# Kernel optimization log

Measured on AMD Instinct MI355X. Metric: run time of the kernel, lower is better.

Reference implementation:

```python
import jax, jax.numpy as jnp
import numpy as np

B, C, IN, OUT = 2048, 64, 512, 512


def setup_inputs() -> dict:
    key = jax.random.key(0)
    k1, k2, k3 = jax.random.split(key, 3)
    x = jax.random.normal(k1, (B, IN), dtype=jnp.float32)
    index = jax.random.randint(k2, (B,), 0, C, dtype=jnp.int64)
    # kaiming_uniform-ish init: bound = sqrt(6 / ((1 + 5) * fan_in)) = 1/sqrt(fan_in)
    bound = 1.0 / np.sqrt(IN)
    weight = jax.random.uniform(k3, (C, OUT, IN), dtype=jnp.float32,
                                minval=-bound, maxval=bound)
    return {"input": x, "index": index, "weight": weight}


def reference(input, index, weight):
    # weight: (C, OUT, IN); index: (B,); input: (B, IN)
    w = weight[index]                      # (B, OUT, IN) gathered per-sample matrix
    return jnp.einsum('boi,bi->bo', w, input)  # batched matvec -> (B, OUT)
```

## Files before the change

kernel.cpp:

```cpp
#include <hip/hip_runtime.h>


constexpr int Bsz  = 2048;
constexpr int Ccnt = 64;
constexpr int INF  = 512;
constexpr int OUTF = 512;
constexpr int THREADS = 256;
constexpr int OT = 64;
constexpr int NT = 64;

typedef __attribute__((ext_vector_type(8))) short bf16x8;
typedef __attribute__((ext_vector_type(4))) float f32x4;

__device__ __forceinline__ unsigned short f2bf(float f) {
    union { float f; unsigned u; } v; v.f = f;
    return (unsigned short)((v.u + 0x7FFFu + ((v.u >> 16) & 1u)) >> 16);
}

__global__ __launch_bounds__(THREADS)
void switching_linear_kernel(const float* __restrict__ x,
                             const int* __restrict__ idx,
                             const float* __restrict__ w,
                             float* __restrict__ out) {
    __shared__ unsigned short list[Bsz];
    __shared__ int ls_n;

    const int tid = threadIdx.x;
    const int c  = blockIdx.x >> 3;
    const int o0 = (blockIdx.x & 7) * OT;

    if (tid == 0) ls_n = 0;
    __syncthreads();
    for (int i = tid; i < Bsz; i += THREADS) {
        if (idx[i] == c) list[atomicAdd(&ls_n, 1)] = (unsigned short)i;
    }
    __syncthreads();
    const int n = ls_n;
    if (n == 0) return;

    const int wave = tid >> 6;
    const int lane = tid & 63;
    const int mrow = lane & 15;
    const int quad = lane >> 4;
    const int ow   = o0 + wave * 16;

    const float* aptr = w + ((size_t)c * OUTF + (size_t)(ow + mrow)) * INF + quad * 8;

    for (int s0 = 0; s0 < n; s0 += NT) {
        const float* bptr[4];
        bool bval[4];
#pragma unroll
        for (int g = 0; g < 4; ++g) {
            int s = s0 + g * 16 + mrow;
            bval[g] = (s < n);
            int b = bval[g] ? (int)list[s] : 0;
            bptr[g] = x + (size_t)b * INF + quad * 8;
        }

        f32x4 acc[4] = {{0.f,0.f,0.f,0.f},{0.f,0.f,0.f,0.f},
                        {0.f,0.f,0.f,0.f},{0.f,0.f,0.f,0.f}};

#pragma unroll 2
        for (int kt = 0; kt < INF; kt += 32) {
            float4 a0 = *(const float4*)(aptr + kt);
            float4 a1 = *(const float4*)(aptr + kt + 4);
            bf16x8 af;
            af[0] = (short)f2bf(a0.x); af[1] = (short)f2bf(a0.y);
            af[2] = (short)f2bf(a0.z); af[3] = (short)f2bf(a0.w);
            af[4] = (short)f2bf(a1.x); af[5] = (short)f2bf(a1.y);
            af[6] = (short)f2bf(a1.z); af[7] = (short)f2bf(a1.w);

#pragma unroll
            for (int g = 0; g < 4; ++g) {
                bf16x8 bf = {0,0,0,0,0,0,0,0};
                if (bval[g]) {
                    float4 b0 = *(const float4*)(bptr[g] + kt);
                    float4 b1 = *(const float4*)(bptr[g] + kt + 4);
                    bf[0] = (short)f2bf(b0.x); bf[1] = (short)f2bf(b0.y);
                    bf[2] = (short)f2bf(b0.z); bf[3] = (short)f2bf(b0.w);
                    bf[4] = (short)f2bf(b1.x); bf[5] = (short)f2bf(b1.y);
                    bf[6] = (short)f2bf(b1.z); bf[7] = (short)f2bf(b1.w);
                }
                acc[g] = __builtin_amdgcn_mfma_f32_16x16x32_bf16(af, bf, acc[g], 0, 0, 0);
            }
        }

#pragma unroll
        for (int g = 0; g < 4; ++g) {
            int s = s0 + g * 16 + mrow;
            if (s < n) {
                int b = (int)list[s];
                float* dst = out + (size_t)b * OUTF + ow + quad * 4;
                *(float4*)dst = make_float4(acc[g][0], acc[g][1], acc[g][2], acc[g][3]);
            }
        }
    }
}

extern "C" void kernel_launch(void* const* d_in, const int* in_sizes, int n_in,
                              void* d_out, int out_size, void* d_ws, size_t ws_size,
                              hipStream_t stream) {
    const float* x   = (const float*)d_in[0];
    const int*   idx = (const int*)d_in[1];
    const float* w   = (const float*)d_in[2];
    float* out = (float*)d_out;

    dim3 grid(Ccnt * (OUTF / OT));
    dim3 block(THREADS);
    switching_linear_kernel<<<grid, block, 0, stream>>>(x, idx, w, out);
}
```

Measured before the change: 125.0 us.

## Split K across waves with LDS reduction, halve output tile, use packed bf16 convert

Halves the output tile per block (doubling the grid to 1024 blocks) and splits the K dimension across wave pairs, combining the two partial sums through shared memory before the store. It also swaps the manual bf16 rounding for a packed hardware conversion builtin when available, and skips MFMA groups that hold no valid samples in the tail tile. The aim is more parallelism and latency hiding for a memory-bound gather GEMM, at the cost of extra syncthreads and LDS traffic per sample tile.

```diff
diff --git a/kernel.cpp b/kernel.cpp
--- a/kernel.cpp
+++ b/kernel.cpp
@@ -6,28 +6,51 @@
 constexpr int INF  = 512;
 constexpr int OUTF = 512;
 constexpr int THREADS = 256;
-constexpr int OT = 64;
+constexpr int OT = 32;
 constexpr int NT = 64;
+constexpr int NBLK = Ccnt * (OUTF / OT);
 
 typedef __attribute__((ext_vector_type(8))) short bf16x8;
 typedef __attribute__((ext_vector_type(4))) float f32x4;
 
-__device__ __forceinline__ unsigned short f2bf(float f) {
+#if __has_builtin(__builtin_amdgcn_cvt_pk_bf16_f32)
+typedef __attribute__((ext_vector_type(2))) __bf16 bf16x2_t;
+__device__ __forceinline__ int cvt2i(float a, float b) {
+    union { bf16x2_t v; int i; } u;
+    u.v = __builtin_amdgcn_cvt_pk_bf16_f32(a, b);
+    return u.i;
+}
+#else
+__device__ __forceinline__ unsigned f2bf(float f) {
     union { float f; unsigned u; } v; v.f = f;
-    return (unsigned short)((v.u + 0x7FFFu + ((v.u >> 16) & 1u)) >> 16);
+    return (v.u + 0x7FFFu + ((v.u >> 16) & 1u)) >> 16;
+}
+__device__ __forceinline__ int cvt2i(float a, float b) {
+    return (int)(f2bf(a) | (f2bf(b) << 16));
+}
+#endif
+
+__device__ __forceinline__ bf16x8 cvt8(float4 a, float4 b) {
+    union { bf16x8 v; int i[4]; } u;
+    u.i[0] = cvt2i(a.x, a.y);
+    u.i[1] = cvt2i(a.z, a.w);
+    u.i[2] = cvt2i(b.x, b.y);
+    u.i[3] = cvt2i(b.z, b.w);
+    return u.v;
 }
 
-__global__ __launch_bounds__(THREADS)
+__global__ __launch_bounds__(THREADS, 4)
 void switching_linear_kernel(const float* __restrict__ x,
                              const int* __restrict__ idx,
                              const float* __restrict__ w,
                              float* __restrict__ out) {
     __shared__ unsigned short list[Bsz];
     __shared__ int ls_n;
+    __shared__ float red[2][16][64];
 
     const int tid = threadIdx.x;
-    const int c  = blockIdx.x >> 3;
-    const int o0 = (blockIdx.x & 7) * OT;
+    const int c  = blockIdx.x >> 4;
+    const int o0 = (blockIdx.x & 15) * OT;
 
     if (tid == 0) ls_n = 0;
     __syncthreads();
@@ -40,13 +63,20 @@
 
     const int wave = tid >> 6;
     const int lane = tid & 63;
+    const int r    = wave & 1;
+    const int kh   = wave >> 1;
     const int mrow = lane & 15;
     const int quad = lane >> 4;
-    const int ow   = o0 + wave * 16;
+    const int ow   = o0 + r * 16;
+    const int k0   = kh * (INF / 2);
 
-    const float* aptr = w + ((size_t)c * OUTF + (size_t)(ow + mrow)) * INF + quad * 8;
+    const float* aptr = w + ((size_t)c * OUTF + (size_t)(ow + mrow)) * INF
+                          + k0 + quad * 8;
 
     for (int s0 = 0; s0 < n; s0 += NT) {
+        const int rem = n - s0;
+        const int ng  = rem >= NT ? 4 : (rem + 15) >> 4;
+
         const float* bptr[4];
         bool bval[4];
 #pragma unroll
@@ -54,46 +84,57 @@
             int s = s0 + g * 16 + mrow;
             bval[g] = (s < n);
             int b = bval[g] ? (int)list[s] : 0;
-            bptr[g] = x + (size_t)b * INF + quad * 8;
+            bptr[g] = x + (size_t)b * INF + k0 + quad * 8;
         }
 
         f32x4 acc[4] = {{0.f,0.f,0.f,0.f},{0.f,0.f,0.f,0.f},
                         {0.f,0.f,0.f,0.f},{0.f,0.f,0.f,0.f}};
 
-#pragma unroll 2
-        for (int kt = 0; kt < INF; kt += 32) {
+#pragma unroll 4
+        for (int kt = 0; kt < INF / 2; kt += 32) {
             float4 a0 = *(const float4*)(aptr + kt);
             float4 a1 = *(const float4*)(aptr + kt + 4);
-            bf16x8 af;
-            af[0] = (short)f2bf(a0.x); af[1] = (short)f2bf(a0.y);
-            af[2] = (short)f2bf(a0.z); af[3] = (short)f2bf(a0.w);
-            af[4] = (short)f2bf(a1.x); af[5] = (short)f2bf(a1.y);
-            af[6] = (short)f2bf(a1.z); af[7] = (short)f2bf(a1.w);
+            bf16x8 af = cvt8(a0, a1);
 
-#pragma unroll
-            for (int g = 0; g < 4; ++g) {
-                bf16x8 bf = {0,0,0,0,0,0,0,0};
+            for (int g = 0; g < ng; ++g) {
+                bf16x8 bfr = {0,0,0,0,0,0,0,0};
                 if (bval[g]) {
                     float4 b0 = *(const float4*)(bptr[g] + kt);
                     float4 b1 = *(const float4*)(bptr[g] + kt + 4);
-                    bf[0] = (short)f2bf(b0.x); bf[1] = (short)f2bf(b0.y);
-                    bf[2] = (short)f2bf(b0.z); bf[3] = (short)f2bf(b0.w);
-                    bf[4] = (short)f2bf(b1.x); bf[5] = (short)f2bf(b1.y);
-                    bf[6] = (short)f2bf(b1.z); bf[7] = (short)f2bf(b1.w);
+                    bfr = cvt8(b0, b1);
                 }
-                acc[g] = __builtin_amdgcn_mfma_f32_16x16x32_bf16(af, bf, acc[g], 0, 0, 0);
+                acc[g] = __builtin_amdgcn_mfma_f32_16x16x32_bf16(af, bfr, acc[g], 0, 0, 0);
             }
         }
 
+        if (kh == 1) {
 #pragma unroll
-        for (int g = 0; g < 4; ++g) {
-            int s = s0 + g * 16 + mrow;
-            if (s < n) {
-                int b = (int)list[s];
-                float* dst = out + (size_t)b * OUTF + ow + quad * 4;
-                *(float4*)dst = make_float4(acc[g][0], acc[g][1], acc[g][2], acc[g][3]);
+            for (int g = 0; g < 4; ++g) {
+                if (g < ng) {
+#pragma unroll
+                    for (int j = 0; j < 4; ++j) red[r][g * 4 + j][lane] = acc[g][j];
+                }
             }
         }
+        __syncthreads();
+        if (kh == 0) {
+#pragma unroll
+            for (int g = 0; g < 4; ++g) {
+                if (g < ng) {
+                    int s = s0 + g * 16 + mrow;
+                    if (s < n) {
+                        float4 v;
+                        v.x = acc[g][0] + red[r][g * 4 + 0][lane];
+                        v.y = acc[g][1] + red[r][g * 4 + 1][lane];
+                        v.z = acc[g][2] + red[r][g * 4 + 2][lane];
+                        v.w = acc[g][3] + red[r][g * 4 + 3][lane];
+                        float* dst = out + (size_t)list[s] * OUTF + ow + quad * 4;
+                        *(float4*)dst = v;
+                    }
+                }
+            }
+        }
+        __syncthreads();
     }
 }
 
@@ -105,7 +146,5 @@
     const float* w   = (const float*)d_in[2];
     float* out = (float*)d_out;
 
-    dim3 grid(Ccnt * (OUTF / OT));
-    dim3 block(THREADS);
-    switching_linear_kernel<<<grid, block, 0, stream>>>(x, idx, w, out);
+    switching_linear_kernel<<<dim3(NBLK), dim3(THREADS), 0, stream>>>(x, idx, w, out);
 }
```

Result: faster. 121.7 us (-2.7%).
